# Kernel optimization log

Hardware: AMD Instinct MI355X
Metric: run time of the kernel (lower is better)

## Reference

```python
import jax, jax.numpy as jnp
import numpy as np
from jax import lax

NUM_CLASSES = 2
PATCH_NUM = 4
TEMP = 0.5
THRESHOLD = 0.6
BDP, FDP = 0.1, 0.9
W_CONTR, W_ENT, W_CONS = 0.1, 0.01, 1.0
RAMP = 40
EPOCH_SEMI = 5
IGNORE = 255


def conv(x, w, stride):
    return lax.conv_general_dilated(x, w, (stride, stride), 'SAME',
                                    dimension_numbers=('NCHW', 'OIHW', 'NCHW'))


def extractor(x, W1, W2, W3):
    h = jax.nn.relu(conv(x, W1, 2))
    h = jax.nn.relu(conv(h, W2, 2))
    return jax.nn.relu(conv(h, W3, 2))  # stride-8 features [B,256,H/8,W/8]


def resize_bilinear_ac(x, oh, ow):
    # bilinear, align_corners=True (matches F.interpolate(..., align_corners=True))
    B, C, H, W = x.shape
    ys = jnp.linspace(0.0, H - 1.0, oh)
    xs = jnp.linspace(0.0, W - 1.0, ow)
    y0 = jnp.floor(ys).astype(jnp.int32); x0 = jnp.floor(xs).astype(jnp.int32)
    y1 = jnp.minimum(y0 + 1, H - 1);      x1 = jnp.minimum(x0 + 1, W - 1)
    wy = (ys - y0)[:, None].astype(x.dtype)
    wx = (xs - x0)[None, :].astype(x.dtype)
    v00 = x[:, :, y0[:, None], x0[None, :]]
    v01 = x[:, :, y0[:, None], x1[None, :]]
    v10 = x[:, :, y1[:, None], x0[None, :]]
    v11 = x[:, :, y1[:, None], x1[None, :]]
    top = v00 * (1 - wx) + v01 * wx
    bot = v10 * (1 - wx) + v11 * wx
    return top * (1 - wy) + bot * wy


def ce_loss(logits, labels, extra_mask=None):
    # logits [B,C,H,W], labels [B,H,W]; mean over valid pixels
    logp = jax.nn.log_softmax(logits, axis=1)
    safe = jnp.clip(labels, 0, logits.shape[1] - 1)
    nll = -jnp.take_along_axis(logp, safe[:, None], axis=1)[:, 0]
    valid = labels != IGNORE
    if extra_mask is not None:
        valid = valid & extra_mask
    valid = valid.astype(logits.dtype)
    return (nll * valid).sum() / jnp.maximum(valid.sum(), 1.0)


def reference(x_l, y_l, x_ul, epoch, proj_ul_ema, z_ul_ema, W1, W2, W3, Wc, bc, Wp):
    # ---- supervised branch ----
    fea_l = extractor(x_l, W1, W2, W3)
    zl_small = conv(fea_l, Wc, 1) + bc[None, :, None, None]
    z_l = resize_bilinear_ac(zl_small, x_l.shape[2], x_l.shape[3])
    loss_sup = ce_loss(z_l, y_l)
    if epoch < EPOCH_SEMI:
        return loss_sup

    # ---- unsupervised branch ----
    fea_ul = extractor(x_ul, W1, W2, W3)
    proj_ul = conv(fea_ul, Wp, 1)
    proj_ul = proj_ul / jnp.maximum(
        jnp.linalg.norm(proj_ul, axis=1, keepdims=True), 1e-12)
    z_ul = conv(fea_ul, Wc, 1) + bc[None, :, None, None]

    # entropy minimization
    logp_ul = jax.nn.log_softmax(z_ul, axis=1)
    p_ul = jnp.exp(logp_ul)
    loss_ent = (-(p_ul * logp_ul).sum(axis=1)).mean()

    pseudo_label = jnp.argmax(z_ul, axis=1)
    p_ema = jax.nn.softmax(z_ul_ema, axis=1)
    max_probs_ema = p_ema.max(axis=1)
    pseudo_label_ema = jnp.argmax(z_ul_ema, axis=1)
    mask_confident = max_probs_ema > THRESHOLD
    loss_cons = ce_loss(z_ul, pseudo_label_ema, mask_confident)

    # ---- vectorized patch extraction (replaces python loops) ----
    B, C, Hp, Wp_ = proj_ul.shape
    P = PATCH_NUM
    h, w = Hp // P, Wp_ // P

    def to_patches(t):  # [B,C,Hp,Wp] -> [P*P*B, h*w, C], torch loop order (j,k,ii)
        return t.reshape(B, C, P, h, P, w).transpose(2, 4, 0, 3, 5, 1).reshape(P * P * B, h * w, C)

    def lab_patches(l):  # [B,Hp,Wp] -> [P*P*B, h*w]
        return l.reshape(B, P, h, P, w).transpose(1, 3, 0, 2, 4).reshape(P * P * B, h * w)

    pat_s = to_patches(proj_ul)
    pat_e = to_patches(proj_ul_ema)
    lab_s = lab_patches(pseudo_label)
    lab_e = lab_patches(pseudo_label_ema)

    feat_all = jnp.concatenate([pat_s.reshape(-1, C), pat_e.reshape(-1, C)], axis=0)  # [M,C]
    lab_all = jnp.concatenate([lab_s.reshape(-1), lab_e.reshape(-1)], axis=0)

    fc = lab_s.astype(proj_ul.dtype).mean(axis=1)  # foreground fraction per patch
    include = jnp.logical_not((fc > BDP) & (fc < FDP)).astype(proj_ul.dtype)

    def patch_loss(anchors, labels_i):  # anchors [hw,C]
        logits = (anchors @ feat_all.T) / TEMP        # [hw, M]
        logp = jax.nn.log_softmax(logits, axis=-1)
        pos = (labels_i[:, None] == lab_all[None, :]).astype(logits.dtype)
        per_anchor = -(pos * logp).sum(-1) / jnp.maximum(pos.sum(-1), 1.0)
        return per_anchor.mean()

    losses = jax.vmap(patch_loss)(pat_s, lab_s)       # [P*P*B]
    loss_contr = (losses * include).sum() / jnp.maximum(include.sum(), 1.0)

    ramp = min(max(epoch / RAMP, 0.0), 1.0)
    cons_w = W_CONS * float(np.exp(-5.0 * (1.0 - ramp) ** 2))

    loss_tot = loss_sup + W_CONTR * loss_contr + cons_w * loss_cons + W_ENT * loss_ent
    return loss_tot


def setup_inputs() -> dict:
    key = jax.random.key(0)
    ks = jax.random.split(key, 12)
    s = 0.05
    return {
        'x_l': jax.random.normal(ks[0], (4, 3, 320, 320), jnp.float32),
        'y_l': jax.random.randint(ks[1], (4, 320, 320), 0, NUM_CLASSES),
        'x_ul': jax.random.normal(ks[2], (4, 3, 320, 320), jnp.float32),
        'epoch': 10,
        'proj_ul_ema': jax.random.normal(ks[3], (4, 128, 40, 40), jnp.float32),
        'z_ul_ema': jax.random.normal(ks[4], (4, 2, 40, 40), jnp.float32),
        'W1': jax.random.normal(ks[5], (64, 3, 3, 3), jnp.float32) * s,
        'W2': jax.random.normal(ks[6], (128, 64, 3, 3), jnp.float32) * s,
        'W3': jax.random.normal(ks[7], (256, 128, 3, 3), jnp.float32) * s,
        'Wc': jax.random.normal(ks[8], (NUM_CLASSES, 256, 1, 1), jnp.float32) * s,
        'bc': jnp.zeros((NUM_CLASSES,), jnp.float32),
        'Wp': jax.random.normal(ks[9], (128, 256, 1, 1), jnp.float32) * s,
    }
```

## Files before the change

### kernel.cpp

```cpp
#include <hip/hip_runtime.h>
#include <math.h>

typedef unsigned short u16;
typedef __attribute__((ext_vector_type(8))) short bf16x8;
typedef __attribute__((ext_vector_type(4))) float f32x4;

static const size_t WS_FEA1B = 0;
static const size_t WS_FEA2B = 6553600;
static const size_t WS_FEA3B = 9830400;
static const size_t WS_ZLS   = 11468800;
static const size_t WS_FEATT = 11481600;
static const size_t WS_LAB   = 13120000;
static const size_t WS_PART  = 13132800;
static const size_t WS_ACC   = 13491200;
static const size_t WS_FC    = 13491216;
static const size_t WS_CSUM  = 13491280;
static const size_t WS_WT2   = 13491536;
static const size_t WS_WT3   = 13528400;
static const size_t WS_WPT   = 13675856;

#define NJS 50


__device__ inline u16 f2bf(float x) {
    unsigned int u = __float_as_uint(x);
    unsigned int r = u + 0x7fffu + ((u >> 16) & 1u);
    return (u16)(r >> 16);
}
__device__ inline float bf2f(u16 v) {
    return __uint_as_float((unsigned int)v << 16);
}

__global__ __launch_bounds__(256) void wtrans(
    const float* __restrict__ W2, const float* __restrict__ W3,
    const float* __restrict__ Wp,
    u16* __restrict__ wt2, u16* __restrict__ wt3, u16* __restrict__ wpt,
    float* __restrict__ accz)
{
    int tid = blockIdx.x * 256 + threadIdx.x;
    if (blockIdx.x == 0) {
        for (int i = threadIdx.x; i < 336; i += 256)
            accz[i] = 0.f;
    }
    if (tid < 73728) {
        int ci = tid & 63, rest = tid >> 6;
        int co = rest & 127, tap = rest >> 7;
        wt2[tid] = f2bf(W2[((size_t)co*64 + ci)*9 + tap]);
    } else if (tid < 368640) {
        int t3 = tid - 73728;
        int ci = t3 & 127, rest = t3 >> 7;
        int co = rest & 255, tap = rest >> 8;
        wt3[t3] = f2bf(W3[((size_t)co*128 + ci)*9 + tap]);
    } else {
        int tp = tid - 368640;
        wpt[tp] = f2bf(Wp[tp]);
    }
}

__global__ __launch_bounds__(256) void conv1_k(
    const float* __restrict__ x_l, const float* __restrict__ x_ul,
    const float* __restrict__ W1, u16* __restrict__ fea1b)
{
    int oy = blockIdx.x;
    int n  = blockIdx.y;
    const float* x = (n < 4) ? x_l + (size_t)n*307200
                             : x_ul + (size_t)(n-4)*307200;
    int t = threadIdx.x;
    int co = t & 63, g = t >> 6;
    __shared__ float lds[9*324];
    for (int u = t; u < 9*322; u += 256) {
        int plane = u / 322, col = u - plane*322;
        int ci = plane / 3, ky = plane - ci*3;
        int iy = oy*2 + ky;
        float v = 0.f;
        if (iy < 320 && col < 320)
            v = x[((size_t)ci*320 + iy)*320 + col];
        lds[plane*324 + col] = v;
    }
    __syncthreads();
    float w[27];
    #pragma unroll
    for (int k = 0; k < 27; ++k) w[k] = W1[co*27 + k];
    float acc[40];
    #pragma unroll
    for (int i = 0; i < 40; ++i) acc[i] = 0.f;
    #pragma unroll
    for (int ci = 0; ci < 3; ++ci) {
        #pragma unroll
        for (int ky = 0; ky < 3; ++ky) {
            const float* base = &lds[(ci*3+ky)*324 + g*80];
            const float* wk = &w[(ci*3+ky)*3];
            #pragma unroll
            for (int q = 0; q < 10; ++q) {
                float4 a = *(const float4*)&base[q*8];
                float4 b = *(const float4*)&base[q*8+4];
                float2 c = *(const float2*)&base[q*8+8];
                float xx[10] = {a.x,a.y,a.z,a.w,b.x,b.y,b.z,b.w,c.x,c.y};
                #pragma unroll
                for (int oo = 0; oo < 4; ++oo)
                    acc[q*4+oo] += wk[0]*xx[2*oo] + wk[1]*xx[2*oo+1] + wk[2]*xx[2*oo+2];
            }
        }
    }
    u16* dst = fea1b + (((size_t)n*160 + oy)*160 + g*40)*64 + co;
    #pragma unroll
    for (int i = 0; i < 40; ++i)
        dst[(size_t)i*64] = f2bf(fmaxf(acc[i], 0.f));
}

template<int Ci, int Co, int H, int OH, int COG>
__global__ __launch_bounds__(256) void conv3x3_nhwc(
    const u16* __restrict__ inb, const u16* __restrict__ wt,
    u16* __restrict__ outb)
{
    constexpr int TILES = OH/8;
    int tile = blockIdx.x;
    int co0  = blockIdx.y * (64*COG);
    int n    = blockIdx.z;
    int ty = tile / TILES, tx = tile - ty*TILES;
    int oy0 = ty*8, ox0 = tx*8;
    int iy0 = oy0*2, ix0 = ox0*2;
    int t = threadIdx.x, lane = t & 63, wv = t >> 6;
    int idx15 = lane & 15, kg = lane >> 4;

    __shared__ u16 lds[306*40];

    f32x4 acc[COG][4];
    #pragma unroll
    for (int cog = 0; cog < COG; ++cog)
        #pragma unroll
        for (int nt = 0; nt < 4; ++nt) acc[cog][nt] = (f32x4){0.f,0.f,0.f,0.f};

    int goff[5], loff[5];
    #pragma unroll
    for (int i = 0; i < 5; ++i) {
        int u = t + i*256;
        if (u < 1224) {
            int pix = u >> 2, q = u & 3;
            int iyl = pix / 18, j = pix - iyl*18;
            int iy = iy0 + iyl, ix = ix0 + j;
            bool ok = (iy < H && ix < H);
            goff[i] = ok ? (((n*H + iy)*H + ix)*Ci + q*8) : -1;
            int jp = (j & 1)*9 + (j >> 1);
            loff[i] = (iyl*18 + jp)*40 + q*8;
        } else goff[i] = -2;
    }
    uint4 vreg[5];
    #pragma unroll
    for (int i = 0; i < 5; ++i) {
        if (goff[i] == -2) continue;
        vreg[i] = (goff[i] >= 0) ? *(const uint4*)&inb[(size_t)goff[i]]
                                 : make_uint4(0,0,0,0);
    }

    for (int c0 = 0; c0 < Ci; c0 += 32) {
        __syncthreads();
        #pragma unroll
        for (int i = 0; i < 5; ++i)
            if (goff[i] != -2) *(uint4*)&lds[loff[i]] = vreg[i];
        __syncthreads();
        if (c0 + 32 < Ci) {
            #pragma unroll
            for (int i = 0; i < 5; ++i) {
                if (goff[i] == -2) continue;
                vreg[i] = (goff[i] >= 0) ? *(const uint4*)&inb[(size_t)goff[i] + c0 + 32]
                                         : make_uint4(0,0,0,0);
            }
        }

        bf16x8 A[COG][9];
        #pragma unroll
        for (int cog = 0; cog < COG; ++cog) {
            const u16* wb = wt + (size_t)(co0 + cog*64 + wv*16 + idx15)*Ci + c0 + kg*8;
            #pragma unroll
            for (int tap = 0; tap < 9; ++tap)
                A[cog][tap] = *(const bf16x8*)(wb + (size_t)tap*Co*Ci);
        }

        #pragma unroll
        for (int tap = 0; tap < 9; ++tap) {
            int ky = tap/3, kx = tap - ky*3;
            #pragma unroll
            for (int nt = 0; nt < 4; ++nt) {
                int l = nt*16 + idx15;
                int iyl = 2*(l>>3) + ky;
                int j = 2*(l&7) + kx;
                int jp = (j&1)*9 + (j>>1);
                bf16x8 B = *(const bf16x8*)&lds[(size_t)(iyl*18 + jp)*40 + kg*8];
                #pragma unroll
                for (int cog = 0; cog < COG; ++cog)
                    acc[cog][nt] = __builtin_amdgcn_mfma_f32_16x16x32_bf16(A[cog][tap], B, acc[cog][nt], 0, 0, 0);
            }
        }
    }

    #pragma unroll
    for (int cog = 0; cog < COG; ++cog) {
        int co = co0 + cog*64 + wv*16 + kg*4;
        #pragma unroll
        for (int nt = 0; nt < 4; ++nt) {
            int l = nt*16 + idx15;
            int oy = oy0 + (l>>3), ox = ox0 + (l&7);
            u16* dst = outb + (((size_t)n*OH + oy)*OH + ox)*Co + co;
            unsigned int p0 = (unsigned int)f2bf(fmaxf(acc[cog][nt][0],0.f))
                            | ((unsigned int)f2bf(fmaxf(acc[cog][nt][1],0.f)) << 16);
            unsigned int p1 = (unsigned int)f2bf(fmaxf(acc[cog][nt][2],0.f))
                            | ((unsigned int)f2bf(fmaxf(acc[cog][nt][3],0.f)) << 16);
            *(uint2*)dst = make_uint2(p0, p1);
        }
    }
}

__global__ __launch_bounds__(256) void cls_ul_fused(
    const u16* __restrict__ feab, const float* __restrict__ Wc,
    const float* __restrict__ bc, const float* __restrict__ z_ema,
    float* __restrict__ zls, int* __restrict__ lab_all,
    float* __restrict__ acc, float* __restrict__ fc_cnt)
{
    int gid = blockIdx.x * 256 + threadIdx.x;
    int px = gid >> 2, part = gid & 3;
    int n = px / 1600, r = px - n*1600;
    const u16* f = feab + (size_t)px * 256 + part*64;
    const float* w0 = Wc + part*64;
    const float* w1 = Wc + 256 + part*64;
    float a0 = 0.f, a1 = 0.f;
    #pragma unroll
    for (int ci = 0; ci < 64; ci += 8) {
        bf16x8 v = *(const bf16x8*)&f[ci];
        #pragma unroll
        for (int j = 0; j < 8; ++j) {
            float x = bf2f((u16)v[j]);
            a0 += x * w0[ci+j];
            a1 += x * w1[ci+j];
        }
    }
    a0 += __shfl_xor(a0, 1); a0 += __shfl_xor(a0, 2);
    a1 += __shfl_xor(a1, 1); a1 += __shfl_xor(a1, 2);

    float ent = 0.f, cn = 0.f, cd = 0.f;
    if (part == 0) {
        if (n < 4) {
            zls[(size_t)n*3200 + r]        = a0;
            zls[(size_t)n*3200 + 1600 + r] = a1;
        } else {
            int nu = n - 4;
            float z0 = a0 + bc[0], z1 = a1 + bc[1];
            float m = fmaxf(z0, z1);
            float e0 = expf(z0 - m), e1 = expf(z1 - m);
            float lse = m + logf(e0 + e1);
            float lp0 = z0 - lse, lp1 = z1 - lse;
            float p0 = expf(lp0), p1 = expf(lp1);
            ent = -(p0*lp0 + p1*lp1);
            int pl = (z1 > z0) ? 1 : 0;
            float ze0 = z_ema[(size_t)nu*3200 + r], ze1 = z_ema[(size_t)nu*3200 + 1600 + r];
            float me = fmaxf(ze0, ze1);
            float f0 = expf(ze0 - me), f1 = expf(ze1 - me);
            float maxp = 1.f / (f0 + f1);
            int ple = (ze1 > ze0) ? 1 : 0;
            bool mask = (maxp > 0.6f);
            float nll = lse - (ple ? z1 : z0);

            int yy = r / 40, xx = r - yy*40;
            int pi = yy / 10, hi = yy % 10, pj = xx / 10, wi = xx % 10;
            int patch = (pi*4 + pj)*4 + nu;
            int row = patch * 100 + hi*10 + wi;
            lab_all[row]        = pl;
            lab_all[6400 + row] = ple;
            atomicAdd(&fc_cnt[patch], (float)pl);
            cn = mask ? nll : 0.f;
            cd = mask ? 1.f : 0.f;
        }
    }
    #pragma unroll
    for (int off = 32; off; off >>= 1) {
        ent += __shfl_down(ent, off);
        cn  += __shfl_down(cn, off);
        cd  += __shfl_down(cd, off);
    }
    if ((threadIdx.x & 63) == 0 && (ent != 0.f || cd != 0.f)) {
        atomicAdd(&acc[2], ent);
        atomicAdd(&acc[3], cn);
        atomicAdd(&acc[4], cd);
    }
}

__global__ __launch_bounds__(256) void loss_sup_kernel(
    const float* __restrict__ zs, const int* __restrict__ y,
    const float* __restrict__ bc, float* __restrict__ acc)
{
    const float step = 39.0f / 319.0f;
    float b0 = bc[0], b1 = bc[1];
    float vn = 0.f, vd = 0.f;
    for (int idx = blockIdx.x*256 + threadIdx.x; idx < 409600; idx += gridDim.x*256) {
        int n  = idx / 102400;
        int r  = idx - n*102400;
        int oy = r / 320, ox = r - oy*320;
        float ty = (float)oy * step, tx = (float)ox * step;
        int y0 = (int)ty, x0 = (int)tx;
        int y1 = min(y0 + 1, 39), x1 = min(x0 + 1, 39);
        float wy = ty - (float)y0, wx = tx - (float)x0;
        const float* base = zs + (size_t)n * 3200;
        float z[2];
        #pragma unroll
        for (int c = 0; c < 2; ++c) {
            const float* pl = base + c * 1600;
            float v00 = pl[y0*40 + x0], v01 = pl[y0*40 + x1];
            float v10 = pl[y1*40 + x0], v11 = pl[y1*40 + x1];
            float top = v00 * (1.f - wx) + v01 * wx;
            float bot = v10 * (1.f - wx) + v11 * wx;
            z[c] = top * (1.f - wy) + bot * wy + (c ? b1 : b0);
        }
        int lab = y[idx];
        bool valid = (lab != 255);
        int sl = min(max(lab, 0), 1);
        float mz  = fmaxf(z[0], z[1]);
        float lse = mz + logf(expf(z[0]-mz) + expf(z[1]-mz));
        float nll = lse - z[sl];
        if (valid) { vn += nll; vd += 1.f; }
    }
    #pragma unroll
    for (int off = 32; off; off >>= 1) { vn += __shfl_down(vn, off); vd += __shfl_down(vd, off); }
    __shared__ float rb[8];
    int wv = threadIdx.x >> 6;
    if ((threadIdx.x & 63) == 0) { rb[wv*2] = vn; rb[wv*2+1] = vd; }
    __syncthreads();
    if (threadIdx.x == 0) {
        atomicAdd(&acc[0], rb[0]+rb[2]+rb[4]+rb[6]);
        atomicAdd(&acc[1], rb[1]+rb[3]+rb[5]+rb[7]);
    }
}

__global__ __launch_bounds__(256) void proj_mfma(
    const u16* __restrict__ fea3b, const u16* __restrict__ wpt,
    u16* __restrict__ featT)
{
    __shared__ float nrm[4][16];
    int b = blockIdx.x;
    int n = b / 100;
    int px0 = (b - n*100) * 16;
    int t = threadIdx.x, lane = t & 63, wv = t >> 6;
    int idx15 = lane & 15, kg = lane >> 4;

    const u16* fb = fea3b + ((size_t)(4+n)*1600 + px0) * 256;

    bf16x8 A[2][8];
    #pragma unroll
    for (int mi = 0; mi < 2; ++mi) {
        const u16* wrow = wpt + (size_t)(wv*32 + mi*16 + idx15)*256 + kg*8;
        #pragma unroll
        for (int ks = 0; ks < 8; ++ks)
            A[mi][ks] = *(const bf16x8*)(wrow + ks*32);
    }

    f32x4 acc[2];
    acc[0] = (f32x4){0.f,0.f,0.f,0.f};
    acc[1] = (f32x4){0.f,0.f,0.f,0.f};

    #pragma unroll
    for (int ks = 0; ks < 8; ++ks) {
        bf16x8 B = *(const bf16x8*)&fb[(size_t)idx15*256 + ks*32 + kg*8];
        acc[0] = __builtin_amdgcn_mfma_f32_16x16x32_bf16(A[0][ks], B, acc[0], 0, 0, 0);
        acc[1] = __builtin_amdgcn_mfma_f32_16x16x32_bf16(A[1][ks], B, acc[1], 0, 0, 0);
    }

    float sq = 0.f;
    #pragma unroll
    for (int mi = 0; mi < 2; ++mi)
        #pragma unroll
        for (int r = 0; r < 4; ++r) sq += acc[mi][r]*acc[mi][r];
    sq += __shfl_xor(sq, 16);
    sq += __shfl_xor(sq, 32);
    if (kg == 0) nrm[wv][idx15] = sq;
    __syncthreads();

    float tot = nrm[0][idx15] + nrm[1][idx15] + nrm[2][idx15] + nrm[3][idx15];
    float scale = 1.f / fmaxf(sqrtf(tot), 1e-12f);
    int rr = px0 + idx15;
    int yy = rr / 40, xx = rr - yy*40;
    int row = ((yy/10*4 + xx/10)*4 + n)*100 + (yy%10)*10 + (xx%10);
    int jt = row >> 4, rl = row & 15;
    u16* base = featT + (size_t)jt*2048;
    #pragma unroll
    for (int mi = 0; mi < 2; ++mi) {
        #pragma unroll
        for (int pr = 0; pr < 2; ++pr) {
            unsigned int pk = (unsigned int)f2bf(acc[mi][2*pr]*scale)
                            | ((unsigned int)f2bf(acc[mi][2*pr+1]*scale) << 16);
            int q = kg*4 + 2*pr;
            int g = wv*4 + mi*2 + (q >> 3);
            *(unsigned int*)&base[(g*16 + rl)*8 + (q & 7)] = pk;
        }
    }
}

__global__ __launch_bounds__(256) void ema_scatter(
    const float* __restrict__ ema, u16* __restrict__ featT,
    unsigned int* __restrict__ maxn)
{
    __shared__ float lds[128*64];
    int b = blockIdx.x;
    int n = b / 25;
    int r0 = (b - n*25) * 64;
    int t = threadIdx.x, lane = t & 63, wv = t >> 6;

    const float* src = ema + ((size_t)n*128 + wv*32)*1600 + r0 + lane;
    int scol = lane ^ (wv << 3);
    #pragma unroll
    for (int cc = 0; cc < 32; ++cc)
        lds[(wv*32 + cc)*64 + scol] = src[(size_t)cc*1600];
    __syncthreads();

    int pxl = t >> 2, cq = t & 3;
    int r = r0 + pxl;
    int yy = r / 40, xx = r - yy*40;
    int row = 6400 + ((yy/10*4 + xx/10)*4 + n)*100 + (yy%10)*10 + (xx%10);
    int rcol = pxl ^ (cq << 3);
    float sq = 0.f;
    unsigned int pk[16];
    #pragma unroll
    for (int i = 0; i < 16; ++i) {
        float v0 = lds[(cq*32 + 2*i)*64 + rcol];
        float v1 = lds[(cq*32 + 2*i + 1)*64 + rcol];
        sq += v0*v0 + v1*v1;
        pk[i] = (unsigned int)f2bf(v0) | ((unsigned int)f2bf(v1) << 16);
    }
    int jt = row >> 4, rl = row & 15;
    u16* base = featT + (size_t)jt*2048;
    #pragma unroll
    for (int k8 = 0; k8 < 4; ++k8) {
        int g = cq*4 + k8;
        *(uint4*)&base[(g*16 + rl)*8] = *(uint4*)&pk[k8*4];
    }

    sq += __shfl_xor(sq, 1);
    sq += __shfl_xor(sq, 2);
    float mx = sq;
    #pragma unroll
    for (int off = 4; off < 64; off <<= 1) mx = fmaxf(mx, __shfl_xor(mx, off));
    __shared__ float red[4];
    if (lane == 0) red[wv] = mx;
    __syncthreads();
    if (t == 0)
        atomicMax(maxn, __float_as_uint(fmaxf(fmaxf(red[0], red[1]),
                                              fmaxf(red[2], red[3]))));
}

__global__ __launch_bounds__(256) void class_sum(
    const u16* __restrict__ featT, const int* __restrict__ lab,
    float* __restrict__ csum, float* __restrict__ acc)
{
    int t = threadIdx.x;
    int chp = t & 63;
    int s   = t >> 6;
    int r0 = blockIdx.x * 100;
    int g = chp >> 2, go = (chp & 3) * 2;
    float s00=0.f, s01=0.f, s10=0.f, s11=0.f;
    float c1 = 0.f;
    for (int i = s; i < 100; i += 4) {
        int row = r0 + i;
        int jt = row >> 4, rl = row & 15;
        unsigned int pk = *(const unsigned int*)&featT[(size_t)jt*2048 + (g*16 + rl)*8 + go];
        float v0 = __uint_as_float(pk << 16);
        float v1 = __uint_as_float(pk & 0xffff0000u);
        int la = lab[row];
        if (la) { s10 += v0; s11 += v1; }
        else    { s00 += v0; s01 += v1; }
        if (chp == 0) c1 += (float)la;
    }
    __shared__ float red[4][256];
    __shared__ float cbuf[4];
    red[s][chp*4+0] = s00; red[s][chp*4+1] = s01;
    red[s][chp*4+2] = s10; red[s][chp*4+3] = s11;
    if (chp == 0) cbuf[s] = c1;
    __syncthreads();
    if (s == 0) {
        #pragma unroll
        for (int k = 0; k < 4; ++k) {
            float v = red[0][chp*4+k] + red[1][chp*4+k] + red[2][chp*4+k] + red[3][chp*4+k];
            int cls = k >> 1, par = k & 1;
            atomicAdd(&csum[cls*128 + 2*chp + par], v);
        }
    }
    if (t == 0)
        atomicAdd(&acc[8], cbuf[0]+cbuf[1]+cbuf[2]+cbuf[3]);
}

__global__ __launch_bounds__(256) void contrast_sE(
    const u16* __restrict__ featT, const unsigned int* __restrict__ maxn,
    float* __restrict__ partials)
{
    int js = blockIdx.x;
    int p0 = blockIdx.y * 2;
    int t = threadIdx.x, lane = t & 63, wv = t >> 6;
    int idx15 = lane & 15;
    int kg = lane >> 4;

    float M = 2.f * sqrtf(__uint_as_float(*maxn)) + 4.f;
    float M2 = M * 1.44269504f;

    bf16x8 A[2][2][4];
    bf16x8 zz = {0,0,0,0,0,0,0,0};
    #pragma unroll
    for (int pi = 0; pi < 2; ++pi) {
        #pragma unroll
        for (int mi = 0; mi < 2; ++mi) {
            int m = wv + mi*4;
            #pragma unroll
            for (int c = 0; c < 4; ++c) {
                int a = 16*m + idx15;
                if (m < 7 && a < 100) {
                    int row = (p0+pi)*100 + a;
                    A[pi][mi][c] = *(const bf16x8*)&featT[
                        (size_t)(row >> 4)*2048 + (((c*4 + kg)*16 + (row & 15)))*8];
                } else A[pi][mi][c] = zz;
            }
        }
    }

    float sE[2][8] = {};
    const u16* jb = featT + (size_t)(js*16)*2048 + (size_t)(kg*16 + idx15)*8;

    bf16x8 Bc[4], Bn[4];
    #pragma unroll
    for (int c = 0; c < 4; ++c)
        Bc[c] = *(const bf16x8*)(jb + c*512);

    for (int jt = 0; jt < 16; ++jt) {
        if (jt < 15) {
            #pragma unroll
            for (int c = 0; c < 4; ++c)
                Bn[c] = *(const bf16x8*)(jb + (size_t)(jt+1)*2048 + c*512);
        }

        #pragma unroll
        for (int pi = 0; pi < 2; ++pi) {
            #pragma unroll
            for (int mi = 0; mi < 2; ++mi) {
                int m = wv + mi*4;
                if (m < 7) {
                    f32x4 C = {0.f, 0.f, 0.f, 0.f};
                    #pragma unroll
                    for (int c = 0; c < 4; ++c)
                        C = __builtin_amdgcn_mfma_f32_16x16x32_bf16(A[pi][mi][c], Bc[c], C, 0, 0, 0);
                    #pragma unroll
                    for (int rr = 0; rr < 4; ++rr)
                        sE[pi][mi*4+rr] += __builtin_amdgcn_exp2f(C[rr] * 2.885390082f - M2);
                }
            }
        }
        #pragma unroll
        for (int c = 0; c < 4; ++c) Bc[c] = Bn[c];
    }

    #pragma unroll
    for (int pi = 0; pi < 2; ++pi) {
        #pragma unroll
        for (int mi = 0; mi < 2; ++mi) {
            int m = wv + mi*4;
            if (m < 7) {
                #pragma unroll
                for (int r = 0; r < 4; ++r) {
                    float s = sE[pi][mi*4+r];
                    #pragma unroll
                    for (int off = 1; off < 16; off <<= 1)
                        s += __shfl_xor(s, off);
                    if (idx15 == 0) {
                        int a = 16*m + 4*kg + r;
                        partials[((size_t)(p0+pi)*NJS + js)*112 + a] = s;
                    }
                }
            }
        }
    }
}

__global__ __launch_bounds__(128) void merge_contrast(
    const float* __restrict__ partials, const float* __restrict__ fc_cnt,
    const unsigned int* __restrict__ maxn, const u16* __restrict__ featT,
    const int* __restrict__ lab, const float* __restrict__ csum,
    float* __restrict__ acc)
{
    int p = blockIdx.x, t = threadIdx.x;
    float pa = 0.f;
    if (t < 100) {
        float s = 0.f;
        for (int js = 0; js < NJS; ++js)
            s += partials[((size_t)p*NJS + js)*112 + t];
        int row = p*100 + t;
        int la = lab[row];
        const float* Sv = csum + la*128;
        int jt = row >> 4, rl = row & 15;
        const u16* base = featT + (size_t)jt*2048;
        float dp = 0.f;
        #pragma unroll
        for (int i = 0; i < 64; ++i) {
            unsigned int pk = *(const unsigned int*)&base[((i >> 2)*16 + rl)*8 + (i & 3)*2];
            dp += __uint_as_float(pk << 16) * Sv[2*i]
                + __uint_as_float(pk & 0xffff0000u) * Sv[2*i+1];
        }
        float N1 = acc[8];
        float cnt = la ? N1 : (12800.f - N1);
        float M = 2.f * sqrtf(__uint_as_float(*maxn)) + 4.f;
        pa = M + logf(s) - 2.f * dp / fmaxf(cnt, 1.f);
    }
    #pragma unroll
    for (int off = 32; off; off >>= 1) pa += __shfl_down(pa, off);
    __shared__ float w2[2];
    if ((t & 63) == 0) w2[t >> 6] = pa;
    __syncthreads();
    if (t == 0) {
        float loss_p = (w2[0] + w2[1]) / 100.f;
        float fcv = fc_cnt[p] / 100.f;
        float inc = ((fcv > 0.1f) && (fcv < 0.9f)) ? 0.f : 1.f;
        atomicAdd(&acc[5], loss_p * inc);
        atomicAdd(&acc[6], inc);
    }
}

__global__ void final_kernel(const float* __restrict__ acc,
                             const int* __restrict__ epoch_p,
                             float* __restrict__ out)
{
    if (threadIdx.x == 0 && blockIdx.x == 0) {
        float loss_sup = acc[0] / fmaxf(acc[1], 1.f);
        int epoch = *epoch_p;
        float loss = loss_sup;
        if (epoch >= 5) {
            float contr = acc[5] / fmaxf(acc[6], 1.f);
            float cons  = acc[3] / fmaxf(acc[4], 1.f);
            float ent   = acc[2] / 6400.f;
            float ramp  = fminf(fmaxf((float)epoch / 40.f, 0.f), 1.f);
            float d = 1.f - ramp;
            float cons_w = expf(-5.f * d * d);
            loss = loss_sup + 0.1f * contr + cons_w * cons + 0.01f * ent;
        }
        out[0] = loss;
    }
}

extern "C" void kernel_launch(void* const* d_in, const int* in_sizes, int n_in,
                              void* d_out, int out_size, void* d_ws, size_t ws_size,
                              hipStream_t stream)
{
    const float* x_l      = (const float*)d_in[0];
    const int*   y_l      = (const int*)  d_in[1];
    const float* x_ul     = (const float*)d_in[2];
    const int*   epoch    = (const int*)  d_in[3];
    const float* proj_ema = (const float*)d_in[4];
    const float* z_ema    = (const float*)d_in[5];
    const float* W1       = (const float*)d_in[6];
    const float* W2       = (const float*)d_in[7];
    const float* W3       = (const float*)d_in[8];
    const float* Wc       = (const float*)d_in[9];
    const float* bc       = (const float*)d_in[10];
    const float* Wp       = (const float*)d_in[11];
    float* out = (float*)d_out;
    float* ws  = (float*)d_ws;

    u16*   fea1b = (u16*)(ws + WS_FEA1B);
    u16*   fea2b = (u16*)(ws + WS_FEA2B);
    u16*   fea3b = (u16*)(ws + WS_FEA3B);
    float* zls   = ws + WS_ZLS;
    u16*   featT = (u16*)(ws + WS_FEATT);
    int*   labA  = (int*)(ws + WS_LAB);
    float* part  = ws + WS_PART;
    float* acc   = ws + WS_ACC;
    float* fc    = ws + WS_FC;
    float* csum  = ws + WS_CSUM;
    u16*   wt2   = (u16*)(ws + WS_WT2);
    u16*   wt3   = (u16*)(ws + WS_WT3);
    u16*   wpt   = (u16*)(ws + WS_WPT);
    unsigned int* maxn = (unsigned int*)(acc + 7);

    wtrans<<<1568, 256, 0, stream>>>(W2, W3, Wp, wt2, wt3, wpt, acc);

    conv1_k<<<dim3(160, 8), 256, 0, stream>>>(x_l, x_ul, W1, fea1b);
    conv3x3_nhwc<64,128,160,80,2><<<dim3(100, 1, 8), 256, 0, stream>>>(fea1b, wt2, fea2b);
    conv3x3_nhwc<128,256,80,40,2><<<dim3(25, 2, 8), 256, 0, stream>>>(fea2b, wt3, fea3b);

    cls_ul_fused<<<200, 256, 0, stream>>>(fea3b, Wc, bc, z_ema, zls, labA, acc, fc);
    loss_sup_kernel<<<512, 256, 0, stream>>>(zls, y_l, bc, acc);

    proj_mfma<<<400, 256, 0, stream>>>(fea3b, wpt, featT);
    ema_scatter<<<100, 256, 0, stream>>>(proj_ema, featT, maxn);
    class_sum<<<128, 256, 0, stream>>>(featT, labA, csum, acc);

    contrast_sE<<<dim3(NJS, 32), 256, 0, stream>>>(featT, maxn, part);
    merge_contrast<<<64, 128, 0, stream>>>(part, fc, maxn, featT, labA, csum, acc);
    final_kernel<<<1, 64, 0, stream>>>(acc, epoch, out);
}
```

Measured before the change: 197.4 us.

## Fold per-class feature sums into proj and EMA scatter kernels, drop class_sum

Removes the separate class_sum kernel. Per-class channel sums are now accumulated with LDS atomics inside proj_mfma and ema_scatter, then added to global csum with one atomic per thread per block. The label-count accumulation (acc[8]) moves into cls_ul_fused. This saves one launch and a re-read of featT. In exchange it adds many shared-memory atomics and sums fp32 values rather than bf16-rounded ones, which slightly changes numerics.

```diff
diff --git a/kernel.cpp b/kernel.cpp
--- a/kernel.cpp
+++ b/kernel.cpp
@@ -237,9 +237,10 @@
     a0 += __shfl_xor(a0, 1); a0 += __shfl_xor(a0, 2);
     a1 += __shfl_xor(a1, 1); a1 += __shfl_xor(a1, 2);
 
-    float ent = 0.f, cn = 0.f, cd = 0.f;
+    bool ul = (n >= 4);
+    float ent = 0.f, cn = 0.f, cd = 0.f, pn = 0.f;
     if (part == 0) {
-        if (n < 4) {
+        if (!ul) {
             zls[(size_t)n*3200 + r]        = a0;
             zls[(size_t)n*3200 + 1600 + r] = a1;
         } else {
@@ -269,6 +270,7 @@
             atomicAdd(&fc_cnt[patch], (float)pl);
             cn = mask ? nll : 0.f;
             cd = mask ? 1.f : 0.f;
+            pn = (float)(pl + ple);
         }
     }
     #pragma unroll
@@ -276,11 +278,13 @@
         ent += __shfl_down(ent, off);
         cn  += __shfl_down(cn, off);
         cd  += __shfl_down(cd, off);
-    }
-    if ((threadIdx.x & 63) == 0 && (ent != 0.f || cd != 0.f)) {
+        pn  += __shfl_down(pn, off);
+    }
+    if ((threadIdx.x & 63) == 0 && ul) {
         atomicAdd(&acc[2], ent);
         atomicAdd(&acc[3], cn);
         atomicAdd(&acc[4], cd);
+        atomicAdd(&acc[8], pn);
     }
 }
 
@@ -332,15 +336,19 @@
 
 __global__ __launch_bounds__(256) void proj_mfma(
     const u16* __restrict__ fea3b, const u16* __restrict__ wpt,
-    u16* __restrict__ featT)
+    const int* __restrict__ lab, u16* __restrict__ featT,
+    float* __restrict__ csum)
 {
     __shared__ float nrm[4][16];
+    __shared__ float cs[256];
     int b = blockIdx.x;
     int n = b / 100;
     int px0 = (b - n*100) * 16;
     int t = threadIdx.x, lane = t & 63, wv = t >> 6;
     int idx15 = lane & 15, kg = lane >> 4;
 
+    cs[t] = 0.f;
+
     const u16* fb = fea3b + ((size_t)(4+n)*1600 + px0) * 256;
 
     bf16x8 A[2][8];
@@ -378,31 +386,41 @@
     int rr = px0 + idx15;
     int yy = rr / 40, xx = rr - yy*40;
     int row = ((yy/10*4 + xx/10)*4 + n)*100 + (yy%10)*10 + (xx%10);
+    int la = lab[row];
     int jt = row >> 4, rl = row & 15;
     u16* base = featT + (size_t)jt*2048;
     #pragma unroll
     for (int mi = 0; mi < 2; ++mi) {
         #pragma unroll
         for (int pr = 0; pr < 2; ++pr) {
-            unsigned int pk = (unsigned int)f2bf(acc[mi][2*pr]*scale)
-                            | ((unsigned int)f2bf(acc[mi][2*pr+1]*scale) << 16);
+            float v0 = acc[mi][2*pr]*scale, v1 = acc[mi][2*pr+1]*scale;
+            unsigned int pk = (unsigned int)f2bf(v0) | ((unsigned int)f2bf(v1) << 16);
             int q = kg*4 + 2*pr;
             int g = wv*4 + mi*2 + (q >> 3);
             *(unsigned int*)&base[(g*16 + rl)*8 + (q & 7)] = pk;
-        }
-    }
+            int ch = wv*32 + mi*16 + q;
+            atomicAdd(&cs[la*128 + ch],     v0);
+            atomicAdd(&cs[la*128 + ch + 1], v1);
+        }
+    }
+    __syncthreads();
+    atomicAdd(&csum[t], cs[t]);
 }
 
 __global__ __launch_bounds__(256) void ema_scatter(
-    const float* __restrict__ ema, u16* __restrict__ featT,
+    const float* __restrict__ ema, const int* __restrict__ lab,
+    u16* __restrict__ featT, float* __restrict__ csum,
     unsigned int* __restrict__ maxn)
 {
     __shared__ float lds[128*64];
+    __shared__ float cs[256];
     int b = blockIdx.x;
     int n = b / 25;
     int r0 = (b - n*25) * 64;
     int t = threadIdx.x, lane = t & 63, wv = t >> 6;
 
+    cs[t] = 0.f;
+
     const float* src = ema + ((size_t)n*128 + wv*32)*1600 + r0 + lane;
     int scol = lane ^ (wv << 3);
     #pragma unroll
@@ -414,6 +432,7 @@
     int r = r0 + pxl;
     int yy = r / 40, xx = r - yy*40;
     int row = 6400 + ((yy/10*4 + xx/10)*4 + n)*100 + (yy%10)*10 + (xx%10);
+    int la = lab[row];
     int rcol = pxl ^ (cq << 3);
     float sq = 0.f;
     unsigned int pk[16];
@@ -423,6 +442,8 @@
         float v1 = lds[(cq*32 + 2*i + 1)*64 + rcol];
         sq += v0*v0 + v1*v1;
         pk[i] = (unsigned int)f2bf(v0) | ((unsigned int)f2bf(v1) << 16);
+        atomicAdd(&cs[la*128 + cq*32 + 2*i],     v0);
+        atomicAdd(&cs[la*128 + cq*32 + 2*i + 1], v1);
     }
     int jt = row >> 4, rl = row & 15;
     u16* base = featT + (size_t)jt*2048;
@@ -443,46 +464,7 @@
     if (t == 0)
         atomicMax(maxn, __float_as_uint(fmaxf(fmaxf(red[0], red[1]),
                                               fmaxf(red[2], red[3]))));
-}
-
-__global__ __launch_bounds__(256) void class_sum(
-    const u16* __restrict__ featT, const int* __restrict__ lab,
-    float* __restrict__ csum, float* __restrict__ acc)
-{
-    int t = threadIdx.x;
-    int chp = t & 63;
-    int s   = t >> 6;
-    int r0 = blockIdx.x * 100;
-    int g = chp >> 2, go = (chp & 3) * 2;
-    float s00=0.f, s01=0.f, s10=0.f, s11=0.f;
-    float c1 = 0.f;
-    for (int i = s; i < 100; i += 4) {
-        int row = r0 + i;
-        int jt = row >> 4, rl = row & 15;
-        unsigned int pk = *(const unsigned int*)&featT[(size_t)jt*2048 + (g*16 + rl)*8 + go];
-        float v0 = __uint_as_float(pk << 16);
-        float v1 = __uint_as_float(pk & 0xffff0000u);
-        int la = lab[row];
-        if (la) { s10 += v0; s11 += v1; }
-        else    { s00 += v0; s01 += v1; }
-        if (chp == 0) c1 += (float)la;
-    }
-    __shared__ float red[4][256];
-    __shared__ float cbuf[4];
-    red[s][chp*4+0] = s00; red[s][chp*4+1] = s01;
-    red[s][chp*4+2] = s10; red[s][chp*4+3] = s11;
-    if (chp == 0) cbuf[s] = c1;
-    __syncthreads();
-    if (s == 0) {
-        #pragma unroll
-        for (int k = 0; k < 4; ++k) {
-            float v = red[0][chp*4+k] + red[1][chp*4+k] + red[2][chp*4+k] + red[3][chp*4+k];
-            int cls = k >> 1, par = k & 1;
-            atomicAdd(&csum[cls*128 + 2*chp + par], v);
-        }
-    }
-    if (t == 0)
-        atomicAdd(&acc[8], cbuf[0]+cbuf[1]+cbuf[2]+cbuf[3]);
+    atomicAdd(&csum[t], cs[t]);
 }
 
 __global__ __launch_bounds__(256) void contrast_sE(
@@ -681,9 +663,8 @@
     cls_ul_fused<<<200, 256, 0, stream>>>(fea3b, Wc, bc, z_ema, zls, labA, acc, fc);
     loss_sup_kernel<<<512, 256, 0, stream>>>(zls, y_l, bc, acc);
 
-    proj_mfma<<<400, 256, 0, stream>>>(fea3b, wpt, featT);
-    ema_scatter<<<100, 256, 0, stream>>>(proj_ema, featT, maxn);
-    class_sum<<<128, 256, 0, stream>>>(featT, labA, csum, acc);
+    proj_mfma<<<400, 256, 0, stream>>>(fea3b, wpt, labA, featT, csum);
+    ema_scatter<<<100, 256, 0, stream>>>(proj_ema, labA, featT, csum, maxn);
 
     contrast_sE<<<dim3(NJS, 32), 256, 0, stream>>>(featT, maxn, part);
     merge_contrast<<<64, 128, 0, stream>>>(part, fc, maxn, featT, labA, csum, acc);
```

After: 210.1 us. 1.06x slower.
